# Performance work log

Hardware: AMD Instinct MI355X
Metric: run time of the kernel (lower is better)

Reference implementation:

```python
import jax, jax.numpy as jnp
import numpy as np
from math import lgamma, log, pi

DIM_Z = 32
KAPPA = 100.0
BATCH = 2048
N_SAMPLES = 32


def _log_iv(v, x, n_terms=300):
    """log of modified Bessel function I_v(x) via stable series (numpy, setup-time only)."""
    ks = np.arange(n_terms)
    logt = (v + 2 * ks) * np.log(x / 2.0) - np.array([lgamma(k + 1.0) + lgamma(v + k + 1.0) for k in ks])
    m = logt.max()
    return float(m + np.log(np.exp(logt - m).sum()))


def _log_C_d(kappa, d):
    """log normalizer of vMF(mu, kappa) on S^{d-1}."""
    v = d / 2.0 - 1.0
    if kappa == 0.0:
        # uniform density on the sphere: 1 / area(S^{d-1})
        return float(lgamma(d / 2.0) - log(2.0) - (d / 2.0) * log(pi))
    return float(v * log(kappa) - (d / 2.0) * log(2.0 * pi) - _log_iv(v, kappa))


def setup_inputs() -> dict:
    key = jax.random.key(0)
    k1, k2 = jax.random.split(key)
    mu = jax.random.normal(k1, (BATCH, DIM_Z), dtype=jnp.float32)
    # approximate vMF(mu, kappa) samples: concentrate noise around normalized mu, project to sphere
    mu_n = mu / jnp.linalg.norm(mu, axis=-1, keepdims=True)
    eps = jax.random.normal(k2, (BATCH, N_SAMPLES, DIM_Z), dtype=jnp.float32)
    z = mu_n[:, None, :] + eps * jnp.float32(1.0 / np.sqrt(KAPPA))
    z = z / jnp.linalg.norm(z, axis=-1, keepdims=True)
    return {
        "mu": mu,
        "z": z,
        "kappa": float(KAPPA),
        "log_C_kappa": _log_C_d(KAPPA, DIM_Z),
        "log_C_zero": _log_C_d(0.0, DIM_Z),
        "n_samples": N_SAMPLES,
    }


def reference(mu, z, kappa, log_C_kappa, log_C_zero, n_samples):
    B, d = mu.shape
    agg_size = B          # agg_size defaults to batch_size
    num_chunks = 1        # B // agg_size
    mu_n = mu / jnp.linalg.norm(mu, axis=-1, keepdims=True)        # [B, d]
    mu_c = mu_n.reshape(num_chunks, agg_size, d)                   # [C, A, d]
    z2 = z.reshape(num_chunks, agg_size * n_samples, d)            # [C, A*n, d]
    # logq[c, i, j] = log vMF_{mu_i}(z_j); avoids the explicit O(A^2 n d) repeat
    logq = jnp.float32(log_C_kappa) + jnp.float32(kappa) * jnp.einsum('cid,cjd->cij', mu_c, z2)
    # exp_mean_log over the component axis i: log mean_i q_i(z_j)
    logq = jax.nn.logsumexp(logq, axis=1) - jnp.log(jnp.float32(agg_size))  # [C, A*n]
    logq = logq.mean(axis=1)                                                # [C]
    okl = (logq - jnp.float32(log_C_zero)).mean(axis=0)
    return okl
```

## Files before the change

### kernel.cpp

```cpp
#include <hip/hip_runtime.h>
#include <hip/hip_bf16.h>


typedef __attribute__((ext_vector_type(8))) short bf16x8;
typedef __attribute__((ext_vector_type(4))) float f32x4;
typedef __attribute__((ext_vector_type(8))) unsigned short u16x8;

#define LOG2E 1.44269504088896340736
#define LN2F 0.6931471805599453f
#define BIAS 48.0
#define MAGIC 1064881816.0
#define CLAMPF 8388608.0f

static __device__ __forceinline__ unsigned short f2bf(float f) {
  unsigned int u = __float_as_uint(f);
  u += 0x7FFFu + ((u >> 16) & 1u);
  return (unsigned short)(u >> 16);
}

__global__ __launch_bounds__(64) void vmf_prep(const float* __restrict__ mu,
                                               const float* __restrict__ kp,
                                               unsigned short* __restrict__ Abf,
                                               int M) {
  int row = blockIdx.x * 64 + threadIdx.x;
  if (row >= M) return;
  const float4* m4 = (const float4*)(mu + (size_t)row * 32);
  float4 v[8];
  float ss = 0.f;
#pragma unroll
  for (int i = 0; i < 8; ++i) {
    v[i] = m4[i];
    ss += v[i].x * v[i].x + v[i].y * v[i].y + v[i].z * v[i].z + v[i].w * v[i].w;
  }
  float sc = (float)((double)kp[0] * LOG2E * 8388608.0) / sqrtf(ss);
  u16x8 o[4];
#pragma unroll
  for (int i = 0; i < 8; ++i) {
    o[i >> 1][(i & 1) * 4 + 0] = f2bf(v[i].x * sc);
    o[i >> 1][(i & 1) * 4 + 1] = f2bf(v[i].y * sc);
    o[i >> 1][(i & 1) * 4 + 2] = f2bf(v[i].z * sc);
    o[i >> 1][(i & 1) * 4 + 3] = f2bf(v[i].w * sc);
  }
  u16x8* dst = (u16x8*)(Abf + (size_t)row * 32);
#pragma unroll
  for (int i = 0; i < 4; ++i) dst[i] = o[i];
}

__global__ __launch_bounds__(512) void vmf_main(const unsigned short* __restrict__ Abf,
                                                const float* __restrict__ z,
                                                const float* __restrict__ kp,
                                                float* __restrict__ part,
                                                int M) {
  const int lane = threadIdx.x & 63;
  const int wave = threadIdx.x >> 6;
  const int r = lane & 15;
  const int q = lane >> 4;
  const float ci = (float)((BIAS - (double)kp[0] * LOG2E) * 8388608.0 + MAGIC);
  const f32x4 cinit = {ci, ci, ci, ci};
  const int colbase = blockIdx.x * 128;

  bf16x8 b[8];
#pragma unroll
  for (int t = 0; t < 8; ++t) {
    const float* zp = z + (size_t)(colbase + t * 16 + r) * 32 + q * 8;
    float4 fa = *(const float4*)zp;
    float4 fb = *(const float4*)(zp + 4);
    b[t][0] = (short)f2bf(fa.x); b[t][1] = (short)f2bf(fa.y);
    b[t][2] = (short)f2bf(fa.z); b[t][3] = (short)f2bf(fa.w);
    b[t][4] = (short)f2bf(fb.x); b[t][5] = (short)f2bf(fb.y);
    b[t][6] = (short)f2bf(fb.z); b[t][7] = (short)f2bf(fb.w);
  }

  const int mchunk = M >> 3;
  const unsigned short* ap = Abf + (size_t)(wave * mchunk + r) * 32 + q * 8;
  bf16x8 av = *(const bf16x8*)ap;
  float acc[8] = {0.f, 0.f, 0.f, 0.f, 0.f, 0.f, 0.f, 0.f};
  for (int m = 0; m < mchunk; m += 16) {
    const int mn = (m + 16) & (mchunk - 1);
    bf16x8 nxt = *(const bf16x8*)(ap + (size_t)mn * 32);
#pragma unroll
    for (int t = 0; t < 8; ++t) {
      f32x4 c = __builtin_amdgcn_mfma_f32_16x16x32_bf16(av, b[t], cinit, 0, 0, 0);
#pragma unroll
      for (int e = 0; e < 4; ++e) {
        float cf = fmaxf(c[e], CLAMPF);
        acc[t] += __int_as_float((int)cf);
      }
    }
    av = nxt;
  }

#pragma unroll
  for (int t = 0; t < 8; ++t) {
    acc[t] += __shfl_xor(acc[t], 16);
    acc[t] += __shfl_xor(acc[t], 32);
  }
  float vlo = (q == 0) ? acc[0] : (q == 1) ? acc[1] : (q == 2) ? acc[2] : acc[3];
  float vhi = (q == 0) ? acc[4] : (q == 1) ? acc[5] : (q == 2) ? acc[6] : acc[7];

  __shared__ float rlo[8][64];
  __shared__ float rhi[8][64];
  rlo[wave][lane] = vlo;
  rhi[wave][lane] = vhi;
  __syncthreads();

  if (wave == 0) {
    float slo = 0.f, shi = 0.f;
#pragma unroll
    for (int w = 0; w < 8; ++w) { slo += rlo[w][lane]; shi += rhi[w][lane]; }
    slo = fmaxf(slo, 1e-38f);
    shi = fmaxf(shi, 1e-38f);
    float t = __logf(slo) + __logf(shi);
    t += __shfl_xor(t, 1);  t += __shfl_xor(t, 2);
    t += __shfl_xor(t, 4);  t += __shfl_xor(t, 8);
    t += __shfl_xor(t, 16); t += __shfl_xor(t, 32);
    if (lane == 0) part[blockIdx.x] = t;
  }
}

__global__ __launch_bounds__(256) void vmf_final(const float* __restrict__ part, int n,
                                                 const float* __restrict__ kp,
                                                 const float* __restrict__ lck,
                                                 const float* __restrict__ lc0,
                                                 float* __restrict__ out,
                                                 int M, int J) {
  __shared__ float red[256];
  float s = 0.f;
  for (int i = threadIdx.x; i < n; i += 256) s += part[i];
  red[threadIdx.x] = s;
  __syncthreads();
  for (int off = 128; off > 0; off >>= 1) {
    if (threadIdx.x < off) red[threadIdx.x] += red[threadIdx.x + off];
    __syncthreads();
  }
  if (threadIdx.x == 0) {
    float tbar = red[0] / (float)J - (float)BIAS * LN2F;
    out[0] = lck[0] + kp[0] + tbar - logf((float)M) - lc0[0];
  }
}

extern "C" void kernel_launch(void* const* d_in, const int* in_sizes, int n_in,
                              void* d_out, int out_size, void* d_ws, size_t ws_size,
                              hipStream_t stream) {
  const float* mu  = (const float*)d_in[0];
  const float* z   = (const float*)d_in[1];
  const float* kp  = (const float*)d_in[2];
  const float* lck = (const float*)d_in[3];
  const float* lc0 = (const float*)d_in[4];
  const int M = in_sizes[0] / 32;
  const int J = in_sizes[1] / 32;

  char* ws = (char*)d_ws;
  unsigned short* Abf = (unsigned short*)ws;
  size_t abytes = ((size_t)M * 32 * 2 + 255) & ~(size_t)255;
  float* part = (float*)(ws + abytes);

  vmf_prep<<<(M + 63) / 64, 64, 0, stream>>>(mu, kp, Abf, M);
  const int nblk = J / 128;
  vmf_main<<<nblk, 512, 0, stream>>>(Abf, z, kp, part, M);
  vmf_final<<<1, 256, 0, stream>>>(part, nblk, kp, lck, lc0, (float*)d_out, M, J);
}
```

Before: 36.77 us.

## Drop final reduction kernel via atomics, widen prep, specialize main loop for M=2048

The separate final reduction launch is removed. The prep kernel now writes the constant terms of the output, and each main block atomically adds its scaled partial sum. The prep kernel spreads each row across 8 threads and combines the squared norms with shuffles. A version of the main kernel specialised for M=2048 fully unrolls the A-fragment loads into double-buffered groups of four, with a generic fallback for other sizes. In exchange, the float atomics make the summation order nondeterministic, and the output initialisation now relies on the prep kernel running before the main kernel on the same stream.

```diff
diff --git a/kernel.cpp b/kernel.cpp
--- a/kernel.cpp
+++ b/kernel.cpp
@@ -4,10 +4,9 @@
 
 typedef __attribute__((ext_vector_type(8))) short bf16x8;
 typedef __attribute__((ext_vector_type(4))) float f32x4;
-typedef __attribute__((ext_vector_type(8))) unsigned short u16x8;
 
 #define LOG2E 1.44269504088896340736
-#define LN2F 0.6931471805599453f
+#define LN2 0.6931471805599453
 #define BIAS 48.0
 #define MAGIC 1064881816.0
 #define CLAMPF 8388608.0f
@@ -18,39 +17,36 @@
   return (unsigned short)(u >> 16);
 }
 
-__global__ __launch_bounds__(64) void vmf_prep(const float* __restrict__ mu,
-                                               const float* __restrict__ kp,
-                                               unsigned short* __restrict__ Abf,
-                                               int M) {
-  int row = blockIdx.x * 64 + threadIdx.x;
+__global__ __launch_bounds__(256) void vmf_prep(const float* __restrict__ mu,
+                                                const float* __restrict__ kp,
+                                                const float* __restrict__ lck,
+                                                const float* __restrict__ lc0,
+                                                unsigned short* __restrict__ Abf,
+                                                float* __restrict__ out, int M) {
+  int tid = blockIdx.x * 256 + threadIdx.x;
+  if (tid == 0) {
+    out[0] = (float)((double)lck[0] + (double)kp[0] - BIAS * LN2 -
+                     log((double)M) - (double)lc0[0]);
+  }
+  int row = tid >> 3;
+  int sub = tid & 7;
   if (row >= M) return;
-  const float4* m4 = (const float4*)(mu + (size_t)row * 32);
-  float4 v[8];
-  float ss = 0.f;
-#pragma unroll
-  for (int i = 0; i < 8; ++i) {
-    v[i] = m4[i];
-    ss += v[i].x * v[i].x + v[i].y * v[i].y + v[i].z * v[i].z + v[i].w * v[i].w;
-  }
+  const float4 v = *(const float4*)(mu + (size_t)row * 32 + sub * 4);
+  float ss = v.x * v.x + v.y * v.y + v.z * v.z + v.w * v.w;
+  ss += __shfl_xor(ss, 1);
+  ss += __shfl_xor(ss, 2);
+  ss += __shfl_xor(ss, 4);
   float sc = (float)((double)kp[0] * LOG2E * 8388608.0) / sqrtf(ss);
-  u16x8 o[4];
-#pragma unroll
-  for (int i = 0; i < 8; ++i) {
-    o[i >> 1][(i & 1) * 4 + 0] = f2bf(v[i].x * sc);
-    o[i >> 1][(i & 1) * 4 + 1] = f2bf(v[i].y * sc);
-    o[i >> 1][(i & 1) * 4 + 2] = f2bf(v[i].z * sc);
-    o[i >> 1][(i & 1) * 4 + 3] = f2bf(v[i].w * sc);
-  }
-  u16x8* dst = (u16x8*)(Abf + (size_t)row * 32);
-#pragma unroll
-  for (int i = 0; i < 4; ++i) dst[i] = o[i];
+  ushort4 o;
+  o.x = f2bf(v.x * sc); o.y = f2bf(v.y * sc);
+  o.z = f2bf(v.z * sc); o.w = f2bf(v.w * sc);
+  *(ushort4*)(Abf + (size_t)row * 32 + sub * 4) = o;
 }
 
 __global__ __launch_bounds__(512) void vmf_main(const unsigned short* __restrict__ Abf,
                                                 const float* __restrict__ z,
                                                 const float* __restrict__ kp,
-                                                float* __restrict__ part,
-                                                int M) {
+                                                float* __restrict__ out, int J) {
   const int lane = threadIdx.x & 63;
   const int wave = threadIdx.x >> 6;
   const int r = lane & 15;
@@ -71,23 +67,33 @@
     b[t][6] = (short)f2bf(fb.z); b[t][7] = (short)f2bf(fb.w);
   }
 
-  const int mchunk = M >> 3;
-  const unsigned short* ap = Abf + (size_t)(wave * mchunk + r) * 32 + q * 8;
-  bf16x8 av = *(const bf16x8*)ap;
+  const unsigned short* ap = Abf + (size_t)(wave * 256 + r) * 32 + q * 8;
   float acc[8] = {0.f, 0.f, 0.f, 0.f, 0.f, 0.f, 0.f, 0.f};
-  for (int m = 0; m < mchunk; m += 16) {
-    const int mn = (m + 16) & (mchunk - 1);
-    bf16x8 nxt = *(const bf16x8*)(ap + (size_t)mn * 32);
-#pragma unroll
-    for (int t = 0; t < 8; ++t) {
-      f32x4 c = __builtin_amdgcn_mfma_f32_16x16x32_bf16(av, b[t], cinit, 0, 0, 0);
-#pragma unroll
-      for (int e = 0; e < 4; ++e) {
-        float cf = fmaxf(c[e], CLAMPF);
-        acc[t] += __int_as_float((int)cf);
+  bf16x8 afA[4], afB[4];
+#pragma unroll
+  for (int f = 0; f < 4; ++f)
+    afA[f] = *(const bf16x8*)(ap + (size_t)(f * 16) * 32);
+#pragma unroll
+  for (int g = 0; g < 4; ++g) {
+    const bf16x8* cur = (g & 1) ? afB : afA;
+    bf16x8* nxt = (g & 1) ? afA : afB;
+    if (g < 3) {
+#pragma unroll
+      for (int f = 0; f < 4; ++f)
+        nxt[f] = *(const bf16x8*)(ap + (size_t)((g + 1) * 64 + f * 16) * 32);
+    }
+#pragma unroll
+    for (int f = 0; f < 4; ++f) {
+#pragma unroll
+      for (int t = 0; t < 8; ++t) {
+        f32x4 c = __builtin_amdgcn_mfma_f32_16x16x32_bf16(cur[f], b[t], cinit, 0, 0, 0);
+#pragma unroll
+        for (int e = 0; e < 4; ++e) {
+          float cf = fmaxf(c[e], CLAMPF);
+          acc[t] += __int_as_float((int)cf);
+        }
       }
     }
-    av = nxt;
   }
 
 #pragma unroll
@@ -114,28 +120,72 @@
     t += __shfl_xor(t, 1);  t += __shfl_xor(t, 2);
     t += __shfl_xor(t, 4);  t += __shfl_xor(t, 8);
     t += __shfl_xor(t, 16); t += __shfl_xor(t, 32);
-    if (lane == 0) part[blockIdx.x] = t;
-  }
-}
-
-__global__ __launch_bounds__(256) void vmf_final(const float* __restrict__ part, int n,
-                                                 const float* __restrict__ kp,
-                                                 const float* __restrict__ lck,
-                                                 const float* __restrict__ lc0,
-                                                 float* __restrict__ out,
-                                                 int M, int J) {
-  __shared__ float red[256];
-  float s = 0.f;
-  for (int i = threadIdx.x; i < n; i += 256) s += part[i];
-  red[threadIdx.x] = s;
+    if (lane == 0) atomicAdd(out, t / (float)J);
+  }
+}
+
+__global__ __launch_bounds__(512) void vmf_main_gen(const unsigned short* __restrict__ Abf,
+                                                    const float* __restrict__ z,
+                                                    const float* __restrict__ kp,
+                                                    float* __restrict__ out,
+                                                    int M, int J) {
+  const int lane = threadIdx.x & 63;
+  const int wave = threadIdx.x >> 6;
+  const int r = lane & 15;
+  const int q = lane >> 4;
+  const float ci = (float)((BIAS - (double)kp[0] * LOG2E) * 8388608.0 + MAGIC);
+  const f32x4 cinit = {ci, ci, ci, ci};
+  const int colbase = blockIdx.x * 128;
+
+  bf16x8 b[8];
+#pragma unroll
+  for (int t = 0; t < 8; ++t) {
+    const float* zp = z + (size_t)(colbase + t * 16 + r) * 32 + q * 8;
+    float4 fa = *(const float4*)zp;
+    float4 fb = *(const float4*)(zp + 4);
+    b[t][0] = (short)f2bf(fa.x); b[t][1] = (short)f2bf(fa.y);
+    b[t][2] = (short)f2bf(fa.z); b[t][3] = (short)f2bf(fa.w);
+    b[t][4] = (short)f2bf(fb.x); b[t][5] = (short)f2bf(fb.y);
+    b[t][6] = (short)f2bf(fb.z); b[t][7] = (short)f2bf(fb.w);
+  }
+
+  float acc[8] = {0.f, 0.f, 0.f, 0.f, 0.f, 0.f, 0.f, 0.f};
+  for (int m = wave * 16; m < M; m += 128) {
+    bf16x8 av = *(const bf16x8*)(Abf + (size_t)(m + r) * 32 + q * 8);
+#pragma unroll
+    for (int t = 0; t < 8; ++t) {
+      f32x4 c = __builtin_amdgcn_mfma_f32_16x16x32_bf16(av, b[t], cinit, 0, 0, 0);
+#pragma unroll
+      for (int e = 0; e < 4; ++e)
+        acc[t] += __int_as_float((int)fmaxf(c[e], CLAMPF));
+    }
+  }
+
+#pragma unroll
+  for (int t = 0; t < 8; ++t) {
+    acc[t] += __shfl_xor(acc[t], 16);
+    acc[t] += __shfl_xor(acc[t], 32);
+  }
+  float vlo = (q == 0) ? acc[0] : (q == 1) ? acc[1] : (q == 2) ? acc[2] : acc[3];
+  float vhi = (q == 0) ? acc[4] : (q == 1) ? acc[5] : (q == 2) ? acc[6] : acc[7];
+
+  __shared__ float rlo[8][64];
+  __shared__ float rhi[8][64];
+  rlo[wave][lane] = vlo;
+  rhi[wave][lane] = vhi;
   __syncthreads();
-  for (int off = 128; off > 0; off >>= 1) {
-    if (threadIdx.x < off) red[threadIdx.x] += red[threadIdx.x + off];
-    __syncthreads();
-  }
-  if (threadIdx.x == 0) {
-    float tbar = red[0] / (float)J - (float)BIAS * LN2F;
-    out[0] = lck[0] + kp[0] + tbar - logf((float)M) - lc0[0];
+
+  if (wave == 0) {
+    float slo = 0.f, shi = 0.f;
+#pragma unroll
+    for (int w = 0; w < 8; ++w) { slo += rlo[w][lane]; shi += rhi[w][lane]; }
+    slo = fmaxf(slo, 1e-38f);
+    shi = fmaxf(shi, 1e-38f);
+    float t = __logf(slo) + __logf(shi);
+    t += __shfl_xor(t, 1);  t += __shfl_xor(t, 2);
+    t += __shfl_xor(t, 4);  t += __shfl_xor(t, 8);
+    t += __shfl_xor(t, 16); t += __shfl_xor(t, 32);
+    if (lane == 0) atomicAdd(out, t / (float)J);
   }
 }
 
@@ -149,14 +199,14 @@
   const float* lc0 = (const float*)d_in[4];
   const int M = in_sizes[0] / 32;
   const int J = in_sizes[1] / 32;
-
-  char* ws = (char*)d_ws;
-  unsigned short* Abf = (unsigned short*)ws;
-  size_t abytes = ((size_t)M * 32 * 2 + 255) & ~(size_t)255;
-  float* part = (float*)(ws + abytes);
-
-  vmf_prep<<<(M + 63) / 64, 64, 0, stream>>>(mu, kp, Abf, M);
+  float* out = (float*)d_out;
+
+  unsigned short* Abf = (unsigned short*)d_ws;
+
+  vmf_prep<<<(M * 8 + 255) / 256, 256, 0, stream>>>(mu, kp, lck, lc0, Abf, out, M);
   const int nblk = J / 128;
-  vmf_main<<<nblk, 512, 0, stream>>>(Abf, z, kp, part, M);
-  vmf_final<<<1, 256, 0, stream>>>(part, nblk, kp, lck, lc0, (float*)d_out, M, J);
-}
+  if (M == 2048)
+    vmf_main<<<nblk, 512, 0, stream>>>(Abf, z, kp, out, J);
+  else
+    vmf_main_gen<<<nblk, 512, 0, stream>>>(Abf, z, kp, out, M, J);
+}
```

Result: no change. 36.46 us (-0.8%).
